# Kernel optimization log

Hardware: AMD Instinct MI355X
Metric: run time of the kernel (lower is better)

## Reference

```python
import jax, jax.numpy as jnp
import numpy as np

B = 4096      # batch
NS = 40       # number of single-valued features (length=1)
NM = 8        # number of multi-valued features
L = 8         # length of each multi-valued feature
V = 10000     # vocab per feature (table rows = V+1, row 0 = padding)
D = 64        # per-feature embedding dim (get_emb_dim(10000,64) == 64)
T = 16        # num_ns_tokens
DM = 512      # d_model
TOTAL = (NS + NM) * D      # 3072, total_emb_dim (pad = 0)
CHUNK = TOTAL // T         # 192, chunk_dim
LN_EPS = 1e-5


def setup_inputs() -> dict:
    key = jax.random.key(0)
    ks = jax.random.split(key, 10)
    int_feats = jax.random.randint(ks[0], (B, NS + NM * L), 0, V + 1)
    emb_single = jax.random.normal(ks[1], (NS, V + 1, D), jnp.float32) * 0.02
    emb_multi = jax.random.normal(ks[2], (NM, V + 1, D), jnp.float32) * 0.02
    h = TOTAL // 4
    lhuc_w1 = jax.random.normal(ks[3], (TOTAL, h), jnp.float32) * 0.02
    lhuc_b1 = jnp.zeros((h,), jnp.float32)
    lhuc_w2 = jax.random.normal(ks[4], (h, TOTAL), jnp.float32) * 0.02
    lhuc_b2 = jnp.zeros((TOTAL,), jnp.float32)
    proj_w = jax.random.normal(ks[5], (T, CHUNK, DM), jnp.float32) * 0.05
    proj_b = jnp.zeros((T, DM), jnp.float32)
    ln_g = jnp.ones((T, DM), jnp.float32)
    ln_b = jnp.zeros((T, DM), jnp.float32)
    return {
        "int_feats": int_feats,
        "emb_single": emb_single, "emb_multi": emb_multi,
        "lhuc_w1": lhuc_w1, "lhuc_b1": lhuc_b1,
        "lhuc_w2": lhuc_w2, "lhuc_b2": lhuc_b2,
        "proj_w": proj_w, "proj_b": proj_b, "ln_g": ln_g, "ln_b": ln_b,
    }


def reference(int_feats, emb_single, emb_multi, lhuc_w1, lhuc_b1,
              lhuc_w2, lhuc_b2, proj_w, proj_b, ln_g, ln_b):
    b = int_feats.shape[0]
    # --- single-valued features: per-feature gather (padding_idx=0 -> zero) ---
    idx_s = int_feats[:, :NS]                                   # (B, NS)
    es = emb_single[jnp.arange(NS)[None, :], idx_s]             # (B, NS, D)
    es = es * (idx_s != 0)[..., None].astype(es.dtype)
    # --- multi-valued features: gather + masked mean pool ---
    idx_m = int_feats[:, NS:].reshape(b, NM, L)                 # (B, NM, L)
    em = emb_multi[jnp.arange(NM)[None, :, None], idx_m]        # (B, NM, L, D)
    mask = (idx_m != 0)[..., None].astype(em.dtype)             # (B, NM, L, 1)
    denom = jnp.maximum(mask.sum(axis=2), 1.0)                  # (B, NM, 1)
    pooled = (em * mask).sum(axis=2) / denom                    # (B, NM, D)
    # --- concat (group order == feature order) ---
    cat = jnp.concatenate([es.reshape(b, NS * D), pooled.reshape(b, NM * D)], axis=-1)  # (B, TOTAL)
    # --- LHUC gating MLP ---
    h = jax.nn.silu(cat @ lhuc_w1 + lhuc_b1)
    gate = jax.nn.sigmoid(h @ lhuc_w2 + lhuc_b2)
    x = (cat * gate * 2.0).reshape(b, T, CHUNK)                 # pad == 0
    # --- per-token Linear + LayerNorm (batched over tokens) ---
    y = jnp.einsum('btc,tcd->btd', x, proj_w) + proj_b          # (B, T, DM)
    mu = y.mean(axis=-1, keepdims=True)
    var = ((y - mu) ** 2).mean(axis=-1, keepdims=True)
    y = (y - mu) * jax.lax.rsqrt(var + LN_EPS) * ln_g + ln_b
    return y
```

## Files before the change

### kernel.cpp

```cpp
#include <hip/hip_runtime.h>
#include <hip/hip_bf16.h>


typedef unsigned short u16;
typedef unsigned int u32;
typedef __attribute__((ext_vector_type(8))) short s16x8;
typedef __attribute__((ext_vector_type(4))) float f32x4;

#define NSF 40
#define NMF 8
#define LLEN 8
#define VROWS 10001
#define DD 64
#define TT 16
#define DMOD 512
#define TOTAL 3072
#define CHUNKC 192
#define NFEAT 104

__device__ __forceinline__ u16 f2bf(float f) {
  __hip_bfloat16 h = __float2bfloat16(f);
  return *reinterpret_cast<u16*>(&h);
}
__device__ __forceinline__ float bf2f(u16 u) {
  __hip_bfloat16 h;
  *reinterpret_cast<u16*>(&h) = u;
  return __bfloat162float(h);
}

__device__ __forceinline__ void gll16(const u16* g, u16* l) {
  __builtin_amdgcn_global_load_lds((const __attribute__((address_space(1))) void*)g,
                                   (__attribute__((address_space(3))) void*)l, 16, 0, 0);
}

__global__ void transpose_cast_kernel(const float* __restrict__ src, u16* __restrict__ dst,
                                      int R, int C, long srcStride, long dstStride) {
  __shared__ float tile[32][33];
  const float* s = src + (long)blockIdx.z * srcStride;
  u16* d = dst + (long)blockIdx.z * dstStride;
  int c0 = blockIdx.x * 32, r0 = blockIdx.y * 32;
#pragma unroll
  for (int i = 0; i < 32; i += 8)
    tile[threadIdx.y + i][threadIdx.x] = s[(long)(r0 + threadIdx.y + i) * C + c0 + threadIdx.x];
  __syncthreads();
#pragma unroll
  for (int i = 0; i < 32; i += 8)
    d[(long)(c0 + threadIdx.y + i) * R + r0 + threadIdx.x] = f2bf(tile[threadIdx.x][threadIdx.y + i]);
}

__global__ __launch_bounds__(256) void embed_kernel(const int* __restrict__ feats,
                                                    const float* __restrict__ tabS,
                                                    const float* __restrict__ tabM,
                                                    u16* __restrict__ catb) {
  int b = blockIdx.x;
  int tid = threadIdx.x;
  int d2 = tid & 31;
  int g = tid >> 5;
  const int* fr = feats + (long)b * NFEAT;
  u16* crow = catb + (long)b * TOTAL;

  for (int f = g; f < NSF; f += 8) {
    int idx = fr[f];
    float x = 0.f, y = 0.f;
    if (idx) {
      const float* e = tabS + ((long)f * VROWS + idx) * DD + d2 * 2;
      x = e[0]; y = e[1];
    }
    u32 pk = (u32)f2bf(x) | ((u32)f2bf(y) << 16);
    *reinterpret_cast<u32*>(crow + f * DD + d2 * 2) = pk;
  }
  int m = g;
  float sx = 0.f, sy = 0.f;
  int cnt = 0;
#pragma unroll
  for (int l = 0; l < LLEN; l++) {
    int idx = fr[NSF + m * LLEN + l];
    if (idx) {
      const float* e = tabM + ((long)m * VROWS + idx) * DD + d2 * 2;
      sx += e[0]; sy += e[1]; cnt++;
    }
  }
  float inv = 1.f / fmaxf((float)cnt, 1.f);
  u32 pk = (u32)f2bf(sx * inv) | ((u32)f2bf(sy * inv) << 16);
  *reinterpret_cast<u32*>(crow + NSF * DD + m * DD + d2 * 2) = pk;
}

template <int N, int K, int BN, int EPI>
__global__ __launch_bounds__(256) void gemm_kernel(const u16* __restrict__ A,
                                                   const u16* __restrict__ Bt,
                                                   const float* __restrict__ bias,
                                                   const u16* __restrict__ aux,
                                                   u16* __restrict__ Out) {
  constexpr int WCOL = BN / 64;
  constexpr int WROW = 4 / WCOL;
  constexpr int MF = (128 / WROW) / 16;
  constexpr int NF = (BN / WCOL) / 16;
  constexpr int NT = K / 32;

  __shared__ u16 lA[2][128 * 32];
  __shared__ u16 lB[2][BN * 32];

  const int tid = threadIdx.x;
  const int w = tid >> 6;
  const int lane = tid & 63;
  const int l15 = lane & 15, hi = lane >> 4;
  const int wr = w / WCOL, wc = w % WCOL;
  const int m0 = blockIdx.y * 128, n0 = blockIdx.x * BN;

  f32x4 acc[MF][NF];
#pragma unroll
  for (int m = 0; m < MF; m++)
#pragma unroll
    for (int n = 0; n < NF; n++) acc[m][n] = (f32x4){0.f, 0.f, 0.f, 0.f};

  const int srow = tid >> 2;
  const int sc8 = (tid & 3) * 8;

  auto stage = [&](int buf, int t) {
    const u16* Ab = A + (long)m0 * K + t * 32;
    const u16* Bb = Bt + (long)n0 * K + t * 32;
#pragma unroll
    for (int i = 0; i < 2; i++)
      gll16(Ab + (long)(i * 64 + srow) * K + sc8, &lA[buf][(i * 256 + w * 64) * 8]);
#pragma unroll
    for (int i = 0; i < BN / 64; i++)
      gll16(Bb + (long)(i * 64 + srow) * K + sc8, &lB[buf][(i * 256 + w * 64) * 8]);
  };

  stage(0, 0);
  __syncthreads();

#pragma unroll 2
  for (int t = 0; t < NT; t++) {
    int buf = t & 1;
    if (t + 1 < NT) stage(buf ^ 1, t + 1);
    s16x8 af[MF], bf[NF];
#pragma unroll
    for (int m = 0; m < MF; m++)
      af[m] = *reinterpret_cast<const s16x8*>(&lA[buf][(wr * (MF * 16) + m * 16 + l15) * 32 + hi * 8]);
#pragma unroll
    for (int n = 0; n < NF; n++)
      bf[n] = *reinterpret_cast<const s16x8*>(&lB[buf][(wc * (NF * 16) + n * 16 + l15) * 32 + hi * 8]);
#pragma unroll
    for (int m = 0; m < MF; m++)
#pragma unroll
      for (int n = 0; n < NF; n++)
        acc[m][n] = __builtin_amdgcn_mfma_f32_16x16x32_bf16(af[m], bf[n], acc[m][n], 0, 0, 0);
    __syncthreads();
  }

#pragma unroll
  for (int n = 0; n < NF; n++) {
    int col = n0 + wc * (NF * 16) + n * 16 + l15;
    float bs = bias[col];
#pragma unroll
    for (int m = 0; m < MF; m++) {
      int rbase = m0 + wr * (MF * 16) + m * 16 + hi * 4;
#pragma unroll
      for (int j = 0; j < 4; j++) {
        int row = rbase + j;
        float z = acc[m][n][j] + bs;
        float o;
        if (EPI == 0) {
          o = z / (1.f + __expf(-z));
        } else {
          float gs = 1.f / (1.f + __expf(-z));
          float xv = bf2f(aux[(long)row * N + col]);
          o = xv * gs * 2.f;
        }
        Out[(long)row * N + col] = f2bf(o);
      }
    }
  }
}

__global__ __launch_bounds__(256) void proj_ln_kernel(const u16* __restrict__ xb,
                                                      const u16* __restrict__ pwt,
                                                      const float* __restrict__ pb,
                                                      const float* __restrict__ lng,
                                                      const float* __restrict__ lnb,
                                                      float* __restrict__ out) {
  __shared__ u16 xs[32][200];
  __shared__ float sred[32][2][2];

  const int t = blockIdx.y;
  const int b0 = blockIdx.x * 32;
  const int tid = threadIdx.x;
  const int w = tid >> 6, lane = tid & 63;
  const int l15 = lane & 15, hi = lane >> 4;
  const int rg = w >> 1, ch = w & 1;

#pragma unroll
  for (int i = 0; i < 3; i++) {
    int chunk = i * 256 + tid;
    int r = chunk / 24, c8 = chunk % 24;
    uint4 v = *reinterpret_cast<const uint4*>(xb + (long)(b0 + r) * TOTAL + t * CHUNKC + c8 * 8);
    *reinterpret_cast<uint4*>(&xs[r][c8 * 8]) = v;
  }
  __syncthreads();

  s16x8 af[6];
#pragma unroll
  for (int kk = 0; kk < 6; kk++)
    af[kk] = *reinterpret_cast<const s16x8*>(&xs[rg * 16 + l15][kk * 32 + hi * 8]);

  f32x4 acc[16];
  const u16* bp = pwt + (long)t * DMOD * CHUNKC + (long)(ch * 256 + l15) * CHUNKC + hi * 8;
#pragma unroll
  for (int n = 0; n < 16; n++) {
    f32x4 a = (f32x4){0.f, 0.f, 0.f, 0.f};
    const u16* bpn = bp + n * 16 * CHUNKC;
#pragma unroll
    for (int kk = 0; kk < 6; kk++) {
      s16x8 bfr = *reinterpret_cast<const s16x8*>(bpn + kk * 32);
      a = __builtin_amdgcn_mfma_f32_16x16x32_bf16(af[kk], bfr, a, 0, 0, 0);
    }
    acc[n] = a;
  }

  float sum[4] = {0, 0, 0, 0}, sq[4] = {0, 0, 0, 0};
#pragma unroll
  for (int n = 0; n < 16; n++) {
    float bs = pb[t * DMOD + ch * 256 + n * 16 + l15];
#pragma unroll
    for (int j = 0; j < 4; j++) {
      float v = acc[n][j] + bs;
      acc[n][j] = v;
      sum[j] += v;
      sq[j] += v * v;
    }
  }
#pragma unroll
  for (int j = 0; j < 4; j++) {
#pragma unroll
    for (int o = 1; o < 16; o <<= 1) {
      sum[j] += __shfl_xor(sum[j], o, 64);
      sq[j] += __shfl_xor(sq[j], o, 64);
    }
  }
  if (l15 == 0) {
#pragma unroll
    for (int j = 0; j < 4; j++) {
      int r = rg * 16 + hi * 4 + j;
      sred[r][ch][0] = sum[j];
      sred[r][ch][1] = sq[j];
    }
  }
  __syncthreads();

  float mean[4], rstd[4];
#pragma unroll
  for (int j = 0; j < 4; j++) {
    int r = rg * 16 + hi * 4 + j;
    float s = sred[r][0][0] + sred[r][1][0];
    float q = sred[r][0][1] + sred[r][1][1];
    float mu = s * (1.f / 512.f);
    float var = q * (1.f / 512.f) - mu * mu;
    mean[j] = mu;
    rstd[j] = rsqrtf(var + 1e-5f);
  }
#pragma unroll
  for (int n = 0; n < 16; n++) {
    int c = ch * 256 + n * 16 + l15;
    float g = lng[t * DMOD + c], bb = lnb[t * DMOD + c];
#pragma unroll
    for (int j = 0; j < 4; j++) {
      int r = rg * 16 + hi * 4 + j;
      float o = (acc[n][j] - mean[j]) * rstd[j] * g + bb;
      out[((long)(b0 + r) * TT + t) * DMOD + c] = o;
    }
  }
}

extern "C" void kernel_launch(void* const* d_in, const int* in_sizes, int n_in,
                              void* d_out, int out_size, void* d_ws, size_t ws_size,
                              hipStream_t stream) {
  const int* feats = (const int*)d_in[0];
  const float* embS = (const float*)d_in[1];
  const float* embM = (const float*)d_in[2];
  const float* w1 = (const float*)d_in[3];
  const float* b1 = (const float*)d_in[4];
  const float* w2 = (const float*)d_in[5];
  const float* b2 = (const float*)d_in[6];
  const float* pw = (const float*)d_in[7];
  const float* pb = (const float*)d_in[8];
  const float* lng = (const float*)d_in[9];
  const float* lnb = (const float*)d_in[10];
  float* out = (float*)d_out;

  char* p = (char*)d_ws;
  u16* catb = (u16*)p; p += (size_t)4096 * 3072 * 2;
  u16* hb   = (u16*)p; p += (size_t)4096 * 768 * 2;
  u16* xb   = (u16*)p; p += (size_t)4096 * 3072 * 2;
  u16* w1t  = (u16*)p; p += (size_t)768 * 3072 * 2;
  u16* w2t  = (u16*)p; p += (size_t)3072 * 768 * 2;
  u16* pwt  = (u16*)p; p += (size_t)16 * 512 * 192 * 2;

  transpose_cast_kernel<<<dim3(768 / 32, 3072 / 32, 1), dim3(32, 8), 0, stream>>>(
      w1, w1t, 3072, 768, 0, 0);
  transpose_cast_kernel<<<dim3(3072 / 32, 768 / 32, 1), dim3(32, 8), 0, stream>>>(
      w2, w2t, 768, 3072, 0, 0);
  transpose_cast_kernel<<<dim3(512 / 32, 192 / 32, 16), dim3(32, 8), 0, stream>>>(
      pw, pwt, 192, 512, 192 * 512, 192 * 512);

  embed_kernel<<<4096, 256, 0, stream>>>(feats, embS, embM, catb);

  gemm_kernel<768, 3072, 64, 0><<<dim3(768 / 64, 4096 / 128), 256, 0, stream>>>(
      catb, w1t, b1, nullptr, hb);

  gemm_kernel<3072, 768, 128, 1><<<dim3(3072 / 128, 4096 / 128), 256, 0, stream>>>(
      hb, w2t, b2, catb, xb);

  proj_ln_kernel<<<dim3(4096 / 32, 16), 256, 0, stream>>>(xb, pwt, pb, lng, lnb, out);
}
```

Baseline: 492.0 us.

## Stage projection weights in LDS and shrink first GEMM tile rows

The per-token projection+LayerNorm kernel is restructured into a 512-thread, 64-row block that double-buffers both activation and weight K-tiles through LDS with async global-to-LDS loads. Previously each wave streamed projection weight fragments straight from global memory. The first LHUC GEMM gets a configurable BM and now uses 64x64 tiles, doubling the grid to improve occupancy and CU fill. The trade-off is more LDS per block and more syncs in the projection kernel, plus lower per-block reuse in the first GEMM.

```diff
diff --git a/kernel.cpp b/kernel.cpp
--- a/kernel.cpp
+++ b/kernel.cpp
@@ -85,19 +85,19 @@
   *reinterpret_cast<u32*>(crow + NSF * DD + m * DD + d2 * 2) = pk;
 }
 
-template <int N, int K, int BN, int EPI>
+template <int N, int K, int BM, int BN, int EPI>
 __global__ __launch_bounds__(256) void gemm_kernel(const u16* __restrict__ A,
                                                    const u16* __restrict__ Bt,
                                                    const float* __restrict__ bias,
                                                    const u16* __restrict__ aux,
                                                    u16* __restrict__ Out) {
-  constexpr int WCOL = BN / 64;
+  constexpr int WCOL = (BN >= 128) ? 2 : 1;
   constexpr int WROW = 4 / WCOL;
-  constexpr int MF = (128 / WROW) / 16;
+  constexpr int MF = (BM / WROW) / 16;
   constexpr int NF = (BN / WCOL) / 16;
   constexpr int NT = K / 32;
 
-  __shared__ u16 lA[2][128 * 32];
+  __shared__ u16 lA[2][BM * 32];
   __shared__ u16 lB[2][BN * 32];
 
   const int tid = threadIdx.x;
@@ -105,7 +105,7 @@
   const int lane = tid & 63;
   const int l15 = lane & 15, hi = lane >> 4;
   const int wr = w / WCOL, wc = w % WCOL;
-  const int m0 = blockIdx.y * 128, n0 = blockIdx.x * BN;
+  const int m0 = blockIdx.y * BM, n0 = blockIdx.x * BN;
 
   f32x4 acc[MF][NF];
 #pragma unroll
@@ -120,7 +120,7 @@
     const u16* Ab = A + (long)m0 * K + t * 32;
     const u16* Bb = Bt + (long)n0 * K + t * 32;
 #pragma unroll
-    for (int i = 0; i < 2; i++)
+    for (int i = 0; i < BM / 64; i++)
       gll16(Ab + (long)(i * 64 + srow) * K + sc8, &lA[buf][(i * 256 + w * 64) * 8]);
 #pragma unroll
     for (int i = 0; i < BN / 64; i++)
@@ -174,101 +174,132 @@
   }
 }
 
-__global__ __launch_bounds__(256) void proj_ln_kernel(const u16* __restrict__ xb,
+__global__ __launch_bounds__(512) void proj_ln_kernel(const u16* __restrict__ xb,
                                                       const u16* __restrict__ pwt,
                                                       const float* __restrict__ pb,
                                                       const float* __restrict__ lng,
                                                       const float* __restrict__ lnb,
                                                       float* __restrict__ out) {
-  __shared__ u16 xs[32][200];
-  __shared__ float sred[32][2][2];
+  __shared__ u16 lA[2][64 * 32];
+  __shared__ u16 lB[2][512 * 32];
+  __shared__ float sred[64][4][2];
 
   const int t = blockIdx.y;
-  const int b0 = blockIdx.x * 32;
+  const int m0 = blockIdx.x * 64;
   const int tid = threadIdx.x;
   const int w = tid >> 6, lane = tid & 63;
   const int l15 = lane & 15, hi = lane >> 4;
-  const int rg = w >> 1, ch = w & 1;
-
-#pragma unroll
-  for (int i = 0; i < 3; i++) {
-    int chunk = i * 256 + tid;
-    int r = chunk / 24, c8 = chunk % 24;
-    uint4 v = *reinterpret_cast<const uint4*>(xb + (long)(b0 + r) * TOTAL + t * CHUNKC + c8 * 8);
-    *reinterpret_cast<uint4*>(&xs[r][c8 * 8]) = v;
-  }
+  const int wr = w >> 2, wc = w & 3;
+
+  const u16* Ab = xb + (long)m0 * TOTAL + t * CHUNKC;
+  const u16* Bb = pwt + (long)t * DMOD * CHUNKC;
+
+  const int srow = tid >> 2;
+  const int sc8 = (tid & 3) * 8;
+
+  auto stage = [&](int buf, int kt) {
+    if (w < 4)
+      gll16(Ab + (long)srow * TOTAL + kt * 32 + sc8, &lA[buf][w * 512]);
+#pragma unroll
+    for (int i = 0; i < 4; i++)
+      gll16(Bb + (long)(i * 128 + srow) * CHUNKC + kt * 32 + sc8,
+            &lB[buf][i * 4096 + w * 512]);
+  };
+
+  f32x4 acc[2][8];
+#pragma unroll
+  for (int m = 0; m < 2; m++)
+#pragma unroll
+    for (int n = 0; n < 8; n++) acc[m][n] = (f32x4){0.f, 0.f, 0.f, 0.f};
+
+  stage(0, 0);
   __syncthreads();
 
-  s16x8 af[6];
-#pragma unroll
-  for (int kk = 0; kk < 6; kk++)
-    af[kk] = *reinterpret_cast<const s16x8*>(&xs[rg * 16 + l15][kk * 32 + hi * 8]);
-
-  f32x4 acc[16];
-  const u16* bp = pwt + (long)t * DMOD * CHUNKC + (long)(ch * 256 + l15) * CHUNKC + hi * 8;
-#pragma unroll
-  for (int n = 0; n < 16; n++) {
-    f32x4 a = (f32x4){0.f, 0.f, 0.f, 0.f};
-    const u16* bpn = bp + n * 16 * CHUNKC;
-#pragma unroll
-    for (int kk = 0; kk < 6; kk++) {
-      s16x8 bfr = *reinterpret_cast<const s16x8*>(bpn + kk * 32);
-      a = __builtin_amdgcn_mfma_f32_16x16x32_bf16(af[kk], bfr, a, 0, 0, 0);
-    }
-    acc[n] = a;
-  }
-
-  float sum[4] = {0, 0, 0, 0}, sq[4] = {0, 0, 0, 0};
-#pragma unroll
-  for (int n = 0; n < 16; n++) {
-    float bs = pb[t * DMOD + ch * 256 + n * 16 + l15];
+#pragma unroll
+  for (int kt = 0; kt < 6; kt++) {
+    int buf = kt & 1;
+    if (kt + 1 < 6) stage(buf ^ 1, kt + 1);
+    s16x8 af[2], bfr[8];
+#pragma unroll
+    for (int m = 0; m < 2; m++)
+      af[m] = *reinterpret_cast<const s16x8*>(&lA[buf][(wr * 32 + m * 16 + l15) * 32 + hi * 8]);
+#pragma unroll
+    for (int n = 0; n < 8; n++)
+      bfr[n] = *reinterpret_cast<const s16x8*>(&lB[buf][(wc * 128 + n * 16 + l15) * 32 + hi * 8]);
+#pragma unroll
+    for (int m = 0; m < 2; m++)
+#pragma unroll
+      for (int n = 0; n < 8; n++)
+        acc[m][n] = __builtin_amdgcn_mfma_f32_16x16x32_bf16(af[m], bfr[n], acc[m][n], 0, 0, 0);
+    __syncthreads();
+  }
+
+  float sum[2][4], sq[2][4];
+#pragma unroll
+  for (int m = 0; m < 2; m++)
+#pragma unroll
+    for (int j = 0; j < 4; j++) { sum[m][j] = 0.f; sq[m][j] = 0.f; }
+
+#pragma unroll
+  for (int n = 0; n < 8; n++) {
+    float bs = pb[t * DMOD + wc * 128 + n * 16 + l15];
+#pragma unroll
+    for (int m = 0; m < 2; m++)
+#pragma unroll
+      for (int j = 0; j < 4; j++) {
+        float v = acc[m][n][j] + bs;
+        acc[m][n][j] = v;
+        sum[m][j] += v;
+        sq[m][j] += v * v;
+      }
+  }
+#pragma unroll
+  for (int m = 0; m < 2; m++)
 #pragma unroll
     for (int j = 0; j < 4; j++) {
-      float v = acc[n][j] + bs;
-      acc[n][j] = v;
-      sum[j] += v;
-      sq[j] += v * v;
-    }
-  }
-#pragma unroll
-  for (int j = 0; j < 4; j++) {
-#pragma unroll
-    for (int o = 1; o < 16; o <<= 1) {
-      sum[j] += __shfl_xor(sum[j], o, 64);
-      sq[j] += __shfl_xor(sq[j], o, 64);
-    }
-  }
+#pragma unroll
+      for (int o = 1; o < 16; o <<= 1) {
+        sum[m][j] += __shfl_xor(sum[m][j], o, 64);
+        sq[m][j] += __shfl_xor(sq[m][j], o, 64);
+      }
+    }
   if (l15 == 0) {
 #pragma unroll
+    for (int m = 0; m < 2; m++)
+#pragma unroll
+      for (int j = 0; j < 4; j++) {
+        int r = wr * 32 + m * 16 + hi * 4 + j;
+        sred[r][wc][0] = sum[m][j];
+        sred[r][wc][1] = sq[m][j];
+      }
+  }
+  __syncthreads();
+
+  float mean[2][4], rstd[2][4];
+#pragma unroll
+  for (int m = 0; m < 2; m++)
+#pragma unroll
     for (int j = 0; j < 4; j++) {
-      int r = rg * 16 + hi * 4 + j;
-      sred[r][ch][0] = sum[j];
-      sred[r][ch][1] = sq[j];
-    }
-  }
-  __syncthreads();
-
-  float mean[4], rstd[4];
-#pragma unroll
-  for (int j = 0; j < 4; j++) {
-    int r = rg * 16 + hi * 4 + j;
-    float s = sred[r][0][0] + sred[r][1][0];
-    float q = sred[r][0][1] + sred[r][1][1];
-    float mu = s * (1.f / 512.f);
-    float var = q * (1.f / 512.f) - mu * mu;
-    mean[j] = mu;
-    rstd[j] = rsqrtf(var + 1e-5f);
-  }
-#pragma unroll
-  for (int n = 0; n < 16; n++) {
-    int c = ch * 256 + n * 16 + l15;
+      int r = wr * 32 + m * 16 + hi * 4 + j;
+      float s = sred[r][0][0] + sred[r][1][0] + sred[r][2][0] + sred[r][3][0];
+      float q = sred[r][0][1] + sred[r][1][1] + sred[r][2][1] + sred[r][3][1];
+      float mu = s * (1.f / 512.f);
+      float var = q * (1.f / 512.f) - mu * mu;
+      mean[m][j] = mu;
+      rstd[m][j] = rsqrtf(var + 1e-5f);
+    }
+#pragma unroll
+  for (int n = 0; n < 8; n++) {
+    int c = wc * 128 + n * 16 + l15;
     float g = lng[t * DMOD + c], bb = lnb[t * DMOD + c];
 #pragma unroll
-    for (int j = 0; j < 4; j++) {
-      int r = rg * 16 + hi * 4 + j;
-      float o = (acc[n][j] - mean[j]) * rstd[j] * g + bb;
-      out[((long)(b0 + r) * TT + t) * DMOD + c] = o;
-    }
+    for (int m = 0; m < 2; m++)
+#pragma unroll
+      for (int j = 0; j < 4; j++) {
+        int r = wr * 32 + m * 16 + hi * 4 + j;
+        float o = (acc[m][n][j] - mean[m][j]) * rstd[m][j] * g + bb;
+        out[((long)(m0 + r) * TT + t) * DMOD + c] = o;
+      }
   }
 }
 
@@ -305,11 +336,11 @@
 
   embed_kernel<<<4096, 256, 0, stream>>>(feats, embS, embM, catb);
 
-  gemm_kernel<768, 3072, 64, 0><<<dim3(768 / 64, 4096 / 128), 256, 0, stream>>>(
+  gemm_kernel<768, 3072, 64, 64, 0><<<dim3(768 / 64, 4096 / 64), 256, 0, stream>>>(
       catb, w1t, b1, nullptr, hb);
 
-  gemm_kernel<3072, 768, 128, 1><<<dim3(3072 / 128, 4096 / 128), 256, 0, stream>>>(
+  gemm_kernel<3072, 768, 128, 128, 1><<<dim3(3072 / 128, 4096 / 128), 256, 0, stream>>>(
       hb, w2t, b2, catb, xb);
 
-  proj_ln_kernel<<<dim3(4096 / 32, 16), 256, 0, stream>>>(xb, pwt, pb, lng, lnb, out);
-}
+  proj_ln_kernel<<<dim3(4096 / 64, 16), 512, 0, stream>>>(xb, pwt, pb, lng, lnb, out);
+}
```

After: 421.5 us. -14.3%, faster.
